# Performance work log

Measured on AMD Instinct MI355X. Metric: run time of the kernel, lower is better.

Reference implementation:

```python
import jax, jax.numpy as jnp
import numpy as np

B, N, H, D, MAXH, MRP = 64, 197, 12, 64, 16, 14  # batch, tokens (14x14+cls), heads, head_dim, supernet max heads, max rel pos
TABLE = 2 * MRP + 2  # 30 rows per table


def setup_inputs() -> dict:
    key = jax.random.key(0)
    ks = jax.random.split(key, 5)
    x = jax.random.normal(ks[0], (B, N, 3 * D * MAXH), dtype=jnp.float32)
    mk = lambda k: (0.02 * jax.random.normal(k, (TABLE, D), dtype=jnp.float32))
    return {"x": x, "tk_v": mk(ks[1]), "tk_h": mk(ks[2]), "tv_v": mk(ks[3]), "tv_h": mk(ks[4])}


def _rel_pos_emb(table_v, table_h, n):
    # RelativePosition2D_super.forward(length_q=n, length_k=n)
    lq = n - 1
    s = int(np.sqrt(lq))  # 14
    r = jnp.arange(lq)
    dv = r[None, :] // s - r[:, None] // s
    dh = r[None, :] % s - r[:, None] % s
    iv = jnp.clip(dv, -MRP, MRP) + MRP + 1
    ih = jnp.clip(dh, -MRP, MRP) + MRP + 1
    iv = jnp.pad(iv, ((1, 0), (1, 0)))  # CLS row/col -> index 0
    ih = jnp.pad(ih, ((1, 0), (1, 0)))
    return table_v[iv] + table_h[ih]  # (n, n, D)


def reference(x, tk_v, tk_h, tv_v, tv_h):
    scale = D ** (-0.5)  # sample_scale = 64**-0.5
    xs = x[:, :, : H * D * 3]
    qkv = xs.reshape(B, N, 3, H, D).transpose(2, 0, 3, 1, 4)  # (3,B,H,N,D)
    q, k, v = qkv[0], qkv[1], qkv[2]
    attn = jnp.einsum('bhid,bhjd->bhij', q, k) * scale
    rk = _rel_pos_emb(tk_v, tk_h, N)  # (N,N,D)
    attn = attn + jnp.einsum('bhid,ijd->bhij', q, rk) * scale
    attn = jax.nn.softmax(attn, axis=-1)  # attn_drop p=0.0 -> identity
    out = jnp.einsum('bhij,bhjd->bhid', attn, v)
    rv = _rel_pos_emb(tv_v, tv_h, N)  # (N,N,D)
    out = out + jnp.einsum('bhij,ijd->bhid', attn, rv)
    out = out.transpose(0, 2, 1, 3).reshape(B, N, H * D)  # (B,N,768)
    return jnp.pad(out, ((0, 0), (0, 0), (0, MAXH * D - H * D)))  # pad to (B,N,1024)
```

## Files before the change

kernel.cpp:

```cpp
#include <hip/hip_runtime.h>

typedef float  f4v   __attribute__((ext_vector_type(4)));
typedef float  f32x4 __attribute__((ext_vector_type(4)));
typedef short  s8v   __attribute__((ext_vector_type(8)));
typedef short  s4v   __attribute__((ext_vector_type(4)));
typedef __bf16 bf16x8 __attribute__((ext_vector_type(8)));

#define N_   197
#define H_   12
#define CIN  3072
#define COUT 1024
#define VSTR 296
#define ASTR 72

#define MEMBAR() asm volatile("" ::: "memory")

__device__ __forceinline__ unsigned short f2bf(float f) {
    unsigned u = __float_as_uint(f);
    u += 0x7FFFu + ((u >> 16) & 1u);
    return (unsigned short)(u >> 16);
}
__device__ __forceinline__ float bf2f(unsigned short s) {
    return __uint_as_float(((unsigned)s) << 16);
}
__device__ __forceinline__ f32x4 mfma_bf16(s8v a, s8v b, f32x4 c) {
    return __builtin_amdgcn_mfma_f32_16x16x32_bf16(
        __builtin_bit_cast(bf16x8, a), __builtin_bit_cast(bf16x8, b), c, 0, 0, 0);
}

__launch_bounds__(1024, 4)
__global__ void attn_super(const float* __restrict__ x,
                           const float* __restrict__ tkv,
                           const float* __restrict__ tkh,
                           const float* __restrict__ tvv,
                           const float* __restrict__ tvh,
                           float* __restrict__ out) {
    __shared__ __align__(16) unsigned short Kl[272 * 72];
    __shared__ __align__(16) unsigned short Vt[64 * VSTR];
    __shared__ __align__(16) unsigned short AR[16][16 * ASTR];
    __shared__ __align__(16) unsigned short INDv[16 * 224];
    __shared__ __align__(16) unsigned short INDh[16 * 224];

    const int bid = blockIdx.x;
    const int b = bid / H_, h = bid % H_;
    const int tid = threadIdx.x;
    const int w  = tid >> 6;
    const int l  = tid & 63;
    const int lg = l >> 4;
    const int ln = l & 15;

    const float* xb = x + (size_t)b * N_ * CIN;

    if (h < 4) {
        float* oz = out + (size_t)b * N_ * COUT + 768 + h * 64;
        for (int idx = tid; idx < N_ * 16; idx += 1024) {
            int row = idx >> 4, c4 = idx & 15;
            f4v z = {0.f, 0.f, 0.f, 0.f};
            *(f4v*)(oz + (size_t)row * COUT + c4 * 4) = z;
        }
    }
    for (int idx = tid; idx < 272 * 16; idx += 1024) {
        int row = idx >> 4, d0 = (idx & 15) * 4;
        f4v v = {0.f, 0.f, 0.f, 0.f};
        if (row < N_)                       v = *(const f4v*)(xb + (size_t)row * CIN + 768 + h * 64 + d0);
        else if (row >= 208 && row < 238)   v = *(const f4v*)(tkv + (row - 208) * 64 + d0);
        else if (row >= 240 && row < 270)   v = *(const f4v*)(tkh + (row - 240) * 64 + d0);
        s4v pk;
        pk[0] = (short)f2bf(v[0]); pk[1] = (short)f2bf(v[1]);
        pk[2] = (short)f2bf(v[2]); pk[3] = (short)f2bf(v[3]);
        *(s4v*)(&Kl[row * 72 + d0]) = pk;
    }
    for (int idx = tid; idx < 288 * 16; idx += 1024) {
        int j = idx % 288, d0 = (idx / 288) * 4;
        f4v v = {0.f, 0.f, 0.f, 0.f};
        if (j < N_)                         v = *(const f4v*)(xb + (size_t)j * CIN + 1536 + h * 64 + d0);
        else if (j >= 224 && j < 254)       v = *(const f4v*)(tvv + (j - 224) * 64 + d0);
        else if (j >= 256 && j < 286)       v = *(const f4v*)(tvh + (j - 256) * 64 + d0);
        #pragma unroll
        for (int e = 0; e < 4; ++e)
            Vt[(d0 + e) * VSTR + j] = f2bf(v[e]);
    }
    for (int idx = tid; idx < 16 * 224; idx += 1024) {
        int m = idx / 224, k = idx % 224;
        int km1 = k - 1;
        bool kv = (k >= 1 && k <= 196);
        INDv[idx] = (kv && (km1 / 14) == m) ? (unsigned short)0x3F80 : (unsigned short)0;
        INDh[idx] = (kv && (km1 % 14) == m) ? (unsigned short)0x3F80 : (unsigned short)0;
    }
    __syncthreads();

    if (w >= 13) return;

    const int tile = w, qb = tile * 16;
    const unsigned short* ar = &AR[w][0];
    volatile unsigned short* arv = &AR[w][0];

    const int iL  = qb + ln;
    const int im1 = (iL > 0) ? iL - 1 : 0;
    const int rit = im1 / 14;
    const int cit = im1 - rit * 14;

    int qrow = qb + ln; if (qrow > 196) qrow = 196;
    const float* qp = xb + (size_t)qrow * CIN + h * 64;
    s8v aq[2];
    #pragma unroll
    for (int s2 = 0; s2 < 2; ++s2) {
        f4v q1 = *(const f4v*)(qp + s2 * 32 + lg * 8);
        f4v q2 = *(const f4v*)(qp + s2 * 32 + lg * 8 + 4);
        #pragma unroll
        for (int e = 0; e < 4; ++e) {
            aq[s2][e]     = (short)f2bf(q1[e] * 0.125f);
            aq[s2][e + 4] = (short)f2bf(q2[e] * 0.125f);
        }
    }
    f32x4 S[13];
    #pragma unroll
    for (int ct = 0; ct < 13; ++ct) {
        f32x4 acc = {0.f, 0.f, 0.f, 0.f};
        #pragma unroll
        for (int s2 = 0; s2 < 2; ++s2) {
            const s8v bk = *(const s8v*)(&Kl[(ct * 16 + ln) * 72 + s2 * 32 + lg * 8]);
            acc = mfma_bf16(bk, aq[s2], acc);
        }
        S[ct] = acc;
    }
    #pragma unroll
    for (int tt = 0; tt < 4; ++tt) {
        f32x4 acc = {0.f, 0.f, 0.f, 0.f};
        #pragma unroll
        for (int s2 = 0; s2 < 2; ++s2) {
            const s8v bk = *(const s8v*)(&Kl[((13 + tt) * 16 + ln) * 72 + s2 * 32 + lg * 8]);
            acc = mfma_bf16(bk, aq[s2], acc);
        }
        #pragma unroll
        for (int r = 0; r < 4; ++r)
            arv[ln * ASTR + tt * 16 + 4 * lg + r] = f2bf(acc[r]);
    }
    MEMBAR();
    if (tile == 0) {
        unsigned short c0  = ar[0];
        unsigned short c32 = ar[32];
        if (l >= 15 && l <= 28) arv[l] = c0;
        if (l >= 47 && l <= 60) arv[l] = c32;
    }
    MEMBAR();
    float rs4[4] = {0.f, 0.f, 0.f, 0.f};
    #pragma unroll
    for (int ct = 0; ct < 13; ++ct) {
        int mj[4], cj[4];
        if (ct == 0) {
            #pragma unroll
            for (int r = 0; r < 4; ++r) {
                int km1 = 4 * lg + r - 1;
                int w14 = (km1 >= 14) ? 1 : 0;
                mj[r] = w14; cj[r] = km1 - 14 * w14;
            }
        } else {
            unsigned e0 = (unsigned)(ct * 16 - 1 + 4 * lg);
            unsigned m0 = e0 / 14u;
            unsigned c0 = e0 - m0 * 14u;
            #pragma unroll
            for (int r = 0; r < 4; ++r) {
                unsigned c = c0 + (unsigned)r;
                int wr = (c >= 14u) ? 1 : 0;
                mj[r] = (int)m0 + wr; cj[r] = (int)c - 14 * wr;
            }
        }
        #pragma unroll
        for (int r = 0; r < 4; ++r) {
            int t = mj[r] - rit + 15;
            int u = cj[r] - cit + 47;
            if (ct == 0 && r == 0) {
                bool z = (lg == 0);
                t = z ? 0 : t;
                u = z ? 32 : u;
            }
            float bias = bf2f(ar[ln * ASTR + t]) + bf2f(ar[ln * ASTR + u]);
            float p = __expf(S[ct][r] + bias);
            if (ct == 12) { if (4 * lg + r > 4) p = 0.f; }
            S[ct][r] = p;
            rs4[r] += p;
        }
    }
    float rs = (rs4[0] + rs4[1]) + (rs4[2] + rs4[3]);
    rs += __shfl_xor(rs, 16);
    rs += __shfl_xor(rs, 32);
    float p00 = S[0][0];
    float rsq[4], p0q[4];
    #pragma unroll
    for (int r = 0; r < 4; ++r) {
        rsq[r] = __shfl(rs,  4 * lg + r);
        p0q[r] = __shfl(p00, 4 * lg + r);
    }
    int ritq[4], citq[4];
    #pragma unroll
    for (int r = 0; r < 4; ++r) {
        int qr2 = qb + 4 * lg + r;
        int im  = (qr2 > 0) ? qr2 - 1 : 0;
        ritq[r] = im / 14;
        citq[r] = im - ritq[r] * 14;
    }
    f32x4 oacc[4];
    #pragma unroll
    for (int nt = 0; nt < 4; ++nt) { f32x4 z = {0.f,0.f,0.f,0.f}; oacc[nt] = z; }
    f32x4 cwv = {0.f,0.f,0.f,0.f}, cwh = {0.f,0.f,0.f,0.f};

    #pragma unroll
    for (int win = 0; win < 3; ++win) {
        MEMBAR();
        #pragma unroll
        for (int cc = 0; cc < 4; ++cc) {
            int ct = win * 4 + cc;
            #pragma unroll
            for (int r = 0; r < 4; ++r)
                arv[ln * ASTR + cc * 16 + 4 * lg + r] = f2bf(S[ct][r]);
        }
        MEMBAR();
        #pragma unroll
        for (int kk = 0; kk < 2; ++kk) {
            int kt = win * 2 + kk;
            const s8v ap = *(const s8v*)(&ar[ln * ASTR + kk * 32 + lg * 8]);
            #pragma unroll
            for (int nt = 0; nt < 4; ++nt) {
                const s8v bv = *(const s8v*)(&Vt[(nt * 16 + ln) * VSTR + kt * 32 + lg * 8]);
                oacc[nt] = mfma_bf16(ap, bv, oacc[nt]);
            }
            const s8v bi = *(const s8v*)(&INDv[ln * 224 + kt * 32 + lg * 8]);
            cwv = mfma_bf16(ap, bi, cwv);
            const s8v bh = *(const s8v*)(&INDh[ln * 224 + kt * 32 + lg * 8]);
            cwh = mfma_bf16(ap, bh, cwh);
        }
    }
    {
        MEMBAR();
        #pragma unroll
        for (int r = 0; r < 4; ++r)
            arv[ln * ASTR + 4 * lg + r] = f2bf(S[12][r]);
        #pragma unroll
        for (int r = 0; r < 4; ++r)
            arv[ln * ASTR + 16 + 4 * lg + r] = 0;
        #pragma unroll
        for (int z = 0; z < 8; ++z)
            arv[ln * ASTR + 32 + lg * 8 + z] = 0;
        MEMBAR();
        {
            const s8v ap = *(const s8v*)(&ar[ln * ASTR + lg * 8]);
            #pragma unroll
            for (int nt = 0; nt < 4; ++nt) {
                const s8v bv = *(const s8v*)(&Vt[(nt * 16 + ln) * VSTR + 192 + lg * 8]);
                oacc[nt] = mfma_bf16(ap, bv, oacc[nt]);
            }
            const s8v bi = *(const s8v*)(&INDv[ln * 224 + 192 + lg * 8]);
            cwv = mfma_bf16(ap, bi, cwv);
            const s8v bh = *(const s8v*)(&INDh[ln * 224 + 192 + lg * 8]);
            cwh = mfma_bf16(ap, bh, cwh);
        }
        MEMBAR();
        #pragma unroll
        for (int r = 0; r < 4; ++r) {
            int q = 4 * lg + r;
            bool isRow0 = (tile == 0) && (q == 0);
            if (ln <= 13 && !isRow0)
                arv[q * ASTR + 47 + ln - ritq[r]] = f2bf(cwv[r]);
            if (ln == 15)
                arv[q * ASTR + 32] = f2bf(isRow0 ? rsq[r] : p0q[r]);
        }
        MEMBAR();
        {
            const s8v ap = *(const s8v*)(&ar[ln * ASTR + 32 + lg * 8]);
            #pragma unroll
            for (int nt = 0; nt < 4; ++nt) {
                const s8v bv = *(const s8v*)(&Vt[(nt * 16 + ln) * VSTR + 224 + lg * 8]);
                oacc[nt] = mfma_bf16(ap, bv, oacc[nt]);
            }
        }
    }
    {
        MEMBAR();
        #pragma unroll
        for (int z = 0; z < 8; ++z)
            arv[ln * ASTR + lg * 8 + z] = 0;
        MEMBAR();
        #pragma unroll
        for (int r = 0; r < 4; ++r) {
            int q = 4 * lg + r;
            bool isRow0 = (tile == 0) && (q == 0);
            if (ln <= 13 && !isRow0)
                arv[q * ASTR + 15 + ln - citq[r]] = f2bf(cwh[r]);
            if (ln == 15)
                arv[q * ASTR + 0] = f2bf(isRow0 ? rsq[r] : p0q[r]);
        }
        MEMBAR();
        {
            const s8v ap = *(const s8v*)(&ar[ln * ASTR + lg * 8]);
            #pragma unroll
            for (int nt = 0; nt < 4; ++nt) {
                const s8v bv = *(const s8v*)(&Vt[(nt * 16 + ln) * VSTR + 256 + lg * 8]);
                oacc[nt] = mfma_bf16(ap, bv, oacc[nt]);
            }
        }
    }
    #pragma unroll
    for (int r = 0; r < 4; ++r) {
        int n = qb + 4 * lg + r;
        if (n < N_) {
            float sc = 1.0f / rsq[r];
            float* orow = out + ((size_t)b * N_ + n) * COUT + h * 64;
            #pragma unroll
            for (int nt = 0; nt < 4; ++nt)
                orow[nt * 16 + ln] = oacc[nt][r] * sc;
        }
    }
}

extern "C" void kernel_launch(void* const* d_in, const int* in_sizes, int n_in,
                              void* d_out, int out_size, void* d_ws, size_t ws_size,
                              hipStream_t stream) {
    const float* x   = (const float*)d_in[0];
    const float* tkv = (const float*)d_in[1];
    const float* tkh = (const float*)d_in[2];
    const float* tvv = (const float*)d_in[3];
    const float* tvh = (const float*)d_in[4];
    float* o = (float*)d_out;
    attn_super<<<dim3(64 * H_), dim3(1024), 0, stream>>>(x, tkv, tkh, tvv, tvh, o);
}
```

Baseline: 76.80 us.

## Batch global loads into registers and overlap V transpose with QK compute

```diff
diff --git a/kernel.cpp b/kernel.cpp
--- a/kernel.cpp
+++ b/kernel.cpp
@@ -26,6 +26,16 @@
 __device__ __forceinline__ f32x4 mfma_bf16(s8v a, s8v b, f32x4 c) {
     return __builtin_amdgcn_mfma_f32_16x16x32_bf16(
         __builtin_bit_cast(bf16x8, a), __builtin_bit_cast(bf16x8, b), c, 0, 0, 0);
+}
+__device__ __forceinline__ void st4f(volatile unsigned short* p, float a, float b, float c, float d) {
+    s4v v;
+    v[0] = (short)f2bf(a); v[1] = (short)f2bf(b);
+    v[2] = (short)f2bf(c); v[3] = (short)f2bf(d);
+    *(volatile s4v*)p = v;
+}
+__device__ __forceinline__ void st4z(volatile unsigned short* p) {
+    s4v v = {0, 0, 0, 0};
+    *(volatile s4v*)p = v;
 }
 
 __launch_bounds__(1024, 4)
@@ -59,26 +69,58 @@
             *(f4v*)(oz + (size_t)row * COUT + c4 * 4) = z;
         }
     }
-    for (int idx = tid; idx < 272 * 16; idx += 1024) {
+
+    f4v kr[5];
+    #pragma unroll
+    for (int it = 0; it < 5; ++it) {
+        int idx = it * 1024 + tid;
+        bool a5 = (it < 4) || (tid < 256);
         int row = idx >> 4, d0 = (idx & 15) * 4;
         f4v v = {0.f, 0.f, 0.f, 0.f};
-        if (row < N_)                       v = *(const f4v*)(xb + (size_t)row * CIN + 768 + h * 64 + d0);
-        else if (row >= 208 && row < 238)   v = *(const f4v*)(tkv + (row - 208) * 64 + d0);
-        else if (row >= 240 && row < 270)   v = *(const f4v*)(tkh + (row - 240) * 64 + d0);
-        s4v pk;
-        pk[0] = (short)f2bf(v[0]); pk[1] = (short)f2bf(v[1]);
-        pk[2] = (short)f2bf(v[2]); pk[3] = (short)f2bf(v[3]);
-        *(s4v*)(&Kl[row * 72 + d0]) = pk;
-    }
-    for (int idx = tid; idx < 288 * 16; idx += 1024) {
+        if (a5) {
+            if (row < N_)                     v = *(const f4v*)(xb + (size_t)row * CIN + 768 + h * 64 + d0);
+            else if (row >= 208 && row < 238) v = *(const f4v*)(tkv + (row - 208) * 64 + d0);
+            else if (row >= 240 && row < 270) v = *(const f4v*)(tkh + (row - 240) * 64 + d0);
+        }
+        kr[it] = v;
+    }
+    f4v q1[2], q2[2];
+    if (w < 13) {
+        int qrow = w * 16 + ln; if (qrow > 196) qrow = 196;
+        const float* qp = xb + (size_t)qrow * CIN + h * 64;
+        #pragma unroll
+        for (int s2 = 0; s2 < 2; ++s2) {
+            q1[s2] = *(const f4v*)(qp + s2 * 32 + lg * 8);
+            q2[s2] = *(const f4v*)(qp + s2 * 32 + lg * 8 + 4);
+        }
+    }
+    f4v vr[5];
+    #pragma unroll
+    for (int it = 0; it < 5; ++it) {
+        int idx = it * 1024 + tid;
+        bool a5 = (it < 4) || (tid < 512);
         int j = idx % 288, d0 = (idx / 288) * 4;
         f4v v = {0.f, 0.f, 0.f, 0.f};
-        if (j < N_)                         v = *(const f4v*)(xb + (size_t)j * CIN + 1536 + h * 64 + d0);
-        else if (j >= 224 && j < 254)       v = *(const f4v*)(tvv + (j - 224) * 64 + d0);
-        else if (j >= 256 && j < 286)       v = *(const f4v*)(tvh + (j - 256) * 64 + d0);
-        #pragma unroll
-        for (int e = 0; e < 4; ++e)
-            Vt[(d0 + e) * VSTR + j] = f2bf(v[e]);
+        if (a5) {
+            if (j < N_)                     v = *(const f4v*)(xb + (size_t)j * CIN + 1536 + h * 64 + d0);
+            else if (j >= 224 && j < 254)   v = *(const f4v*)(tvv + (j - 224) * 64 + d0);
+            else if (j >= 256 && j < 286)   v = *(const f4v*)(tvh + (j - 256) * 64 + d0);
+        }
+        vr[it] = v;
+    }
+
+    #pragma unroll
+    for (int it = 0; it < 5; ++it) {
+        int idx = it * 1024 + tid;
+        bool a5 = (it < 4) || (tid < 256);
+        if (a5) {
+            int row = idx >> 4, d0 = (idx & 15) * 4;
+            f4v v = kr[it];
+            s4v pk;
+            pk[0] = (short)f2bf(v[0]); pk[1] = (short)f2bf(v[1]);
+            pk[2] = (short)f2bf(v[2]); pk[3] = (short)f2bf(v[3]);
+            *(s4v*)(&Kl[row * 72 + d0]) = pk;
+        }
     }
     for (int idx = tid; idx < 16 * 224; idx += 1024) {
         int m = idx / 224, k = idx % 224;
@@ -89,117 +131,129 @@
     }
     __syncthreads();
 
-    if (w >= 13) return;
-
     const int tile = w, qb = tile * 16;
     const unsigned short* ar = &AR[w][0];
     volatile unsigned short* arv = &AR[w][0];
 
-    const int iL  = qb + ln;
-    const int im1 = (iL > 0) ? iL - 1 : 0;
-    const int rit = im1 / 14;
-    const int cit = im1 - rit * 14;
-
-    int qrow = qb + ln; if (qrow > 196) qrow = 196;
-    const float* qp = xb + (size_t)qrow * CIN + h * 64;
-    s8v aq[2];
-    #pragma unroll
-    for (int s2 = 0; s2 < 2; ++s2) {
-        f4v q1 = *(const f4v*)(qp + s2 * 32 + lg * 8);
-        f4v q2 = *(const f4v*)(qp + s2 * 32 + lg * 8 + 4);
-        #pragma unroll
-        for (int e = 0; e < 4; ++e) {
-            aq[s2][e]     = (short)f2bf(q1[e] * 0.125f);
-            aq[s2][e + 4] = (short)f2bf(q2[e] * 0.125f);
-        }
-    }
     f32x4 S[13];
-    #pragma unroll
-    for (int ct = 0; ct < 13; ++ct) {
-        f32x4 acc = {0.f, 0.f, 0.f, 0.f};
+    if (w < 13) {
+        s8v aq[2];
         #pragma unroll
         for (int s2 = 0; s2 < 2; ++s2) {
-            const s8v bk = *(const s8v*)(&Kl[(ct * 16 + ln) * 72 + s2 * 32 + lg * 8]);
-            acc = mfma_bf16(bk, aq[s2], acc);
-        }
-        S[ct] = acc;
-    }
-    #pragma unroll
-    for (int tt = 0; tt < 4; ++tt) {
-        f32x4 acc = {0.f, 0.f, 0.f, 0.f};
-        #pragma unroll
-        for (int s2 = 0; s2 < 2; ++s2) {
-            const s8v bk = *(const s8v*)(&Kl[((13 + tt) * 16 + ln) * 72 + s2 * 32 + lg * 8]);
-            acc = mfma_bf16(bk, aq[s2], acc);
-        }
-        #pragma unroll
-        for (int r = 0; r < 4; ++r)
-            arv[ln * ASTR + tt * 16 + 4 * lg + r] = f2bf(acc[r]);
-    }
-    MEMBAR();
-    if (tile == 0) {
-        unsigned short c0  = ar[0];
-        unsigned short c32 = ar[32];
-        if (l >= 15 && l <= 28) arv[l] = c0;
-        if (l >= 47 && l <= 60) arv[l] = c32;
-    }
-    MEMBAR();
-    float rs4[4] = {0.f, 0.f, 0.f, 0.f};
-    #pragma unroll
-    for (int ct = 0; ct < 13; ++ct) {
-        int mj[4], cj[4];
-        if (ct == 0) {
+            #pragma unroll
+            for (int e = 0; e < 4; ++e) {
+                aq[s2][e]     = (short)f2bf(q1[s2][e] * 0.125f);
+                aq[s2][e + 4] = (short)f2bf(q2[s2][e] * 0.125f);
+            }
+        }
+        #pragma unroll
+        for (int ct = 0; ct < 13; ++ct) {
+            f32x4 acc = {0.f, 0.f, 0.f, 0.f};
+            #pragma unroll
+            for (int s2 = 0; s2 < 2; ++s2) {
+                const s8v bk = *(const s8v*)(&Kl[(ct * 16 + ln) * 72 + s2 * 32 + lg * 8]);
+                acc = mfma_bf16(bk, aq[s2], acc);
+            }
+            S[ct] = acc;
+        }
+        #pragma unroll
+        for (int tt = 0; tt < 4; ++tt) {
+            f32x4 acc = {0.f, 0.f, 0.f, 0.f};
+            #pragma unroll
+            for (int s2 = 0; s2 < 2; ++s2) {
+                const s8v bk = *(const s8v*)(&Kl[((13 + tt) * 16 + ln) * 72 + s2 * 32 + lg * 8]);
+                acc = mfma_bf16(bk, aq[s2], acc);
+            }
+            st4f(&arv[ln * ASTR + tt * 16 + 4 * lg], acc[0], acc[1], acc[2], acc[3]);
+        }
+    }
+    #pragma unroll
+    for (int it = 0; it < 5; ++it) {
+        int idx = it * 1024 + tid;
+        bool a5 = (it < 4) || (tid < 512);
+        if (a5) {
+            int j = idx % 288, d0 = (idx / 288) * 4;
+            f4v v = vr[it];
+            #pragma unroll
+            for (int e = 0; e < 4; ++e)
+                Vt[(d0 + e) * VSTR + j] = f2bf(v[e]);
+        }
+    }
+
+    float rsq[4], p0q[4];
+    int ritq[4], citq[4];
+    if (w < 13) {
+        MEMBAR();
+        if (tile == 0) {
+            unsigned short c0  = ar[0];
+            unsigned short c32 = ar[32];
+            if (l >= 15 && l <= 28) arv[l] = c0;
+            if (l >= 47 && l <= 60) arv[l] = c32;
+        }
+        MEMBAR();
+        const int iL  = qb + ln;
+        const int im1 = (iL > 0) ? iL - 1 : 0;
+        const int rit = im1 / 14;
+        const int cit = im1 - rit * 14;
+        float rs4[4] = {0.f, 0.f, 0.f, 0.f};
+        #pragma unroll
+        for (int ct = 0; ct < 13; ++ct) {
+            int mj[4], cj[4];
+            if (ct == 0) {
+                #pragma unroll
+                for (int r = 0; r < 4; ++r) {
+                    int km1 = 4 * lg + r - 1;
+                    int w14 = (km1 >= 14) ? 1 : 0;
+                    mj[r] = w14; cj[r] = km1 - 14 * w14;
+                }
+            } else {
+                unsigned e0 = (unsigned)(ct * 16 - 1 + 4 * lg);
+                unsigned m0 = e0 / 14u;
+                unsigned c0 = e0 - m0 * 14u;
+                #pragma unroll
+                for (int r = 0; r < 4; ++r) {
+                    unsigned c = c0 + (unsigned)r;
+                    int wr = (c >= 14u) ? 1 : 0;
+                    mj[r] = (int)m0 + wr; cj[r] = (int)c - 14 * wr;
+                }
+            }
             #pragma unroll
             for (int r = 0; r < 4; ++r) {
-                int km1 = 4 * lg + r - 1;
-                int w14 = (km1 >= 14) ? 1 : 0;
-                mj[r] = w14; cj[r] = km1 - 14 * w14;
-            }
-        } else {
-            unsigned e0 = (unsigned)(ct * 16 - 1 + 4 * lg);
-            unsigned m0 = e0 / 14u;
-            unsigned c0 = e0 - m0 * 14u;
-            #pragma unroll
-            for (int r = 0; r < 4; ++r) {
-                unsigned c = c0 + (unsigned)r;
-                int wr = (c >= 14u) ? 1 : 0;
-                mj[r] = (int)m0 + wr; cj[r] = (int)c - 14 * wr;
-            }
-        }
+                int t = mj[r] - rit + 15;
+                int u = cj[r] - cit + 47;
+                if (ct == 0 && r == 0) {
+                    bool z = (lg == 0);
+                    t = z ? 0 : t;
+                    u = z ? 32 : u;
+                }
+                float bias = bf2f(ar[ln * ASTR + t]) + bf2f(ar[ln * ASTR + u]);
+                float p = __expf(S[ct][r] + bias);
+                if (ct == 12) { if (4 * lg + r > 4) p = 0.f; }
+                S[ct][r] = p;
+                rs4[r] += p;
+            }
+        }
+        float rs = (rs4[0] + rs4[1]) + (rs4[2] + rs4[3]);
+        rs += __shfl_xor(rs, 16);
+        rs += __shfl_xor(rs, 32);
+        float p00 = S[0][0];
         #pragma unroll
         for (int r = 0; r < 4; ++r) {
-            int t = mj[r] - rit + 15;
-            int u = cj[r] - cit + 47;
-            if (ct == 0 && r == 0) {
-                bool z = (lg == 0);
-                t = z ? 0 : t;
-                u = z ? 32 : u;
-            }
-            float bias = bf2f(ar[ln * ASTR + t]) + bf2f(ar[ln * ASTR + u]);
-            float p = __expf(S[ct][r] + bias);
-            if (ct == 12) { if (4 * lg + r > 4) p = 0.f; }
-            S[ct][r] = p;
-            rs4[r] += p;
-        }
-    }
-    float rs = (rs4[0] + rs4[1]) + (rs4[2] + rs4[3]);
-    rs += __shfl_xor(rs, 16);
-    rs += __shfl_xor(rs, 32);
-    float p00 = S[0][0];
-    float rsq[4], p0q[4];
-    #pragma unroll
-    for (int r = 0; r < 4; ++r) {
-        rsq[r] = __shfl(rs,  4 * lg + r);
-        p0q[r] = __shfl(p00, 4 * lg + r);
-    }
-    int ritq[4], citq[4];
-    #pragma unroll
-    for (int r = 0; r < 4; ++r) {
-        int qr2 = qb + 4 * lg + r;
-        int im  = (qr2 > 0) ? qr2 - 1 : 0;
-        ritq[r] = im / 14;
-        citq[r] = im - ritq[r] * 14;
-    }
+            rsq[r] = __shfl(rs,  4 * lg + r);
+            p0q[r] = __shfl(p00, 4 * lg + r);
+        }
+        #pragma unroll
+        for (int r = 0; r < 4; ++r) {
+            int qr2 = qb + 4 * lg + r;
+            int im  = (qr2 > 0) ? qr2 - 1 : 0;
+            ritq[r] = im / 14;
+            citq[r] = im - ritq[r] * 14;
+        }
+    }
+    __syncthreads();
+
+    if (w >= 13) return;
+
     f32x4 oacc[4];
     #pragma unroll
     for (int nt = 0; nt < 4; ++nt) { f32x4 z = {0.f,0.f,0.f,0.f}; oacc[nt] = z; }
@@ -211,9 +265,7 @@
         #pragma unroll
         for (int cc = 0; cc < 4; ++cc) {
             int ct = win * 4 + cc;
-            #pragma unroll
-            for (int r = 0; r < 4; ++r)
-                arv[ln * ASTR + cc * 16 + 4 * lg + r] = f2bf(S[ct][r]);
+            st4f(&arv[ln * ASTR + cc * 16 + 4 * lg], S[ct][0], S[ct][1], S[ct][2], S[ct][3]);
         }
         MEMBAR();
         #pragma unroll
@@ -233,15 +285,10 @@
     }
     {
         MEMBAR();
-        #pragma unroll
-        for (int r = 0; r < 4; ++r)
-            arv[ln * ASTR + 4 * lg + r] = f2bf(S[12][r]);
-        #pragma unroll
-        for (int r = 0; r < 4; ++r)
-            arv[ln * ASTR + 16 + 4 * lg + r] = 0;
-        #pragma unroll
-        for (int z = 0; z < 8; ++z)
-            arv[ln * ASTR + 32 + lg * 8 + z] = 0;
+        st4f(&arv[ln * ASTR + 4 * lg], S[12][0], S[12][1], S[12][2], S[12][3]);
+        st4z(&arv[ln * ASTR + 16 + 4 * lg]);
+        st4z(&arv[ln * ASTR + 32 + lg * 8]);
+        st4z(&arv[ln * ASTR + 36 + lg * 8]);
         MEMBAR();
         {
             const s8v ap = *(const s8v*)(&ar[ln * ASTR + lg * 8]);
@@ -277,9 +324,8 @@
     }
     {
         MEMBAR();
-        #pragma unroll
-        for (int z = 0; z < 8; ++z)
-            arv[ln * ASTR + lg * 8 + z] = 0;
+        st4z(&arv[ln * ASTR + lg * 8]);
+        st4z(&arv[ln * ASTR + 4 + lg * 8]);
         MEMBAR();
         #pragma unroll
         for (int r = 0; r < 4; ++r) {
```

Result: no change. 75.34 us (-1.9%).
